# Kernel optimization log

Measured on AMD Instinct MI355X. Metric: run time of the kernel, lower is better.

The kernel has to match this reference:

```python
import jax, jax.numpy as jnp
from jax import lax
import numpy as np

B, N, G, K = 4, 1024, 128, 32
D_MODEL, DEPTH, CLS = 384, 12, 40
D_INNER, D_STATE, D_CONV, DT_RANK = 768, 16, 4, 24
EPS = 1e-5
BN_SCALE = 1.0 / float(np.sqrt(1.0 + EPS))  # eval BN, running_mean=0, running_var=1


def layernorm(x, w, b):
    mu = x.mean(-1, keepdims=True)
    var = ((x - mu) ** 2).mean(-1, keepdims=True)
    return (x - mu) * lax.rsqrt(var + EPS) * w + b


def bn_eval(x, g, b):
    return x * (g * BN_SCALE) + b


def fps(xyz, n):
    Bb, Nn, _ = xyz.shape
    first = jnp.zeros((Bb,), jnp.int32)

    def step(carry, _):
        dmin, last = carry
        p = jnp.take_along_axis(xyz, last[:, None, None], axis=1)  # B,1,3
        dmin = jnp.minimum(dmin, jnp.sum((xyz - p) ** 2, -1))
        nxt = jnp.argmax(dmin, -1).astype(jnp.int32)
        return (dmin, nxt), nxt

    _, rest = lax.scan(step, (jnp.full((Bb, Nn), 1e10, xyz.dtype), first), None, length=n - 1)
    return jnp.concatenate([first[None, :], rest], 0).T  # B,G


def group_points(xyz):
    idx = fps(xyz, G)
    center = jnp.take_along_axis(xyz, idx[:, :, None], axis=1)            # B,G,3
    d2 = jnp.sum((center[:, :, None, :] - xyz[:, None, :, :]) ** 2, -1)   # B,G,N
    _, knn = lax.top_k(-d2, K)                                            # B,G,K
    nb = jax.vmap(lambda p, i: p[i])(xyz, knn)                            # B,G,K,3
    return nb - center[:, :, None, :], center


def encoder(pg, w1, b1, g1, bb1, w2, b2, w3, b3, g2, bb2, w4, b4):
    Bb, Gg, Kk, _ = pg.shape
    f = pg.reshape(Bb * Gg, Kk, 3)
    f = jax.nn.relu(bn_eval(f @ w1.T + b1, g1, bb1))                      # BG,K,128
    f = f @ w2.T + b2                                                     # BG,K,256
    fg = f.max(1, keepdims=True)
    f = jnp.concatenate([jnp.broadcast_to(fg, f.shape), f], -1)           # BG,K,512
    f = jax.nn.relu(bn_eval(f @ w3.T + b3, g2, bb2))
    f = f @ w4.T + b4
    return f.max(1).reshape(Bb, Gg, -1)                                   # B,G,C


def mamba_mixer(x, ipw, cw, cb, xpw, dpw, dpb, A_log, Dp, opw):
    L = x.shape[1]
    xz = x @ ipw.T                                                        # B,L,2*Di
    u, z = jnp.split(xz, 2, -1)
    up = jnp.pad(u, ((0, 0), (D_CONV - 1, 0), (0, 0)))                    # causal depthwise conv
    u = sum(up[:, k:k + L, :] * cw[:, k] for k in range(D_CONV)) + cb
    u = jax.nn.silu(u)
    xdb = u @ xpw.T
    dt, Bm, Cm = jnp.split(xdb, [DT_RANK, DT_RANK + D_STATE], -1)
    dt = jax.nn.softplus(dt @ dpw.T + dpb)                                # B,L,Di
    A = -jnp.exp(A_log)                                                   # Di,Ds

    def step(h, inp):
        dt_t, B_t, C_t, u_t = inp
        h = jnp.exp(dt_t[:, :, None] * A) * h + (dt_t * u_t)[:, :, None] * B_t[:, None, :]
        return h, jnp.einsum('bds,bs->bd', h, C_t)

    h0 = jnp.zeros((x.shape[0], D_INNER, D_STATE), x.dtype)
    _, ys = lax.scan(step, h0, (dt.swapaxes(0, 1), Bm.swapaxes(0, 1), Cm.swapaxes(0, 1), u.swapaxes(0, 1)))
    y = ys.swapaxes(0, 1) + u * Dp
    return (y * jax.nn.silu(z)) @ opw.T


def forward(pts, enc_w1, enc_b1, enc_bn1_g, enc_bn1_b, enc_w2, enc_b2, enc_w3, enc_b3,
            enc_bn2_g, enc_bn2_b, enc_w4, enc_b4, pos_w1, pos_b1, pos_w2, pos_b2,
            ln_w, ln_b, in_proj_w, conv_w, conv_b, x_proj_w, dt_proj_w, dt_proj_b,
            A_log, D_param, out_proj_w, normf_w, normf_b, norm_w, norm_b,
            head_w1, head_b1, head_bn1_g, head_bn1_b, head_w2, head_b2,
            head_bn2_g, head_bn2_b, head_w3, head_b3):
    nb, center = group_points(pts)
    tok = encoder(nb, enc_w1, enc_b1, enc_bn1_g, enc_bn1_b, enc_w2, enc_b2,
                  enc_w3, enc_b3, enc_bn2_g, enc_bn2_b, enc_w4, enc_b4)    # B,G,384
    pos = jax.nn.gelu(center @ pos_w1.T + pos_b1, approximate=False) @ pos_w2.T + pos_b2

    # PointMamba token reordering: sort by center x, y, z and concatenate -> L = 3G
    toks, poss = [], []
    for ax in range(3):
        o = jnp.argsort(center[:, :, ax], axis=-1)[:, :, None]
        toks.append(jnp.take_along_axis(tok, o, axis=1))
        poss.append(jnp.take_along_axis(pos, o, axis=1))
    tok = jnp.concatenate(toks, 1)
    pos = jnp.concatenate(poss, 1)

    h = tok + pos
    res = jnp.zeros_like(h)

    def layer_step(carry, p):
        h, res = carry
        lnw, lnb, ipw, cw, cb, xpw, dpw, dpb, Al, Dp, opw = p
        res = h + res
        x = layernorm(res, lnw, lnb)
        h = mamba_mixer(x, ipw, cw, cb, xpw, dpw, dpb, Al, Dp, opw)
        return (h, res), None

    (h, res), _ = lax.scan(layer_step, (h, res),
                           (ln_w, ln_b, in_proj_w, conv_w, conv_b, x_proj_w,
                            dt_proj_w, dt_proj_b, A_log, D_param, out_proj_w))
    x = layernorm(h + res, normf_w, normf_b)   # MixerModel.norm_f
    x = layernorm(x, norm_w, norm_b)           # PointMamba.norm
    feat = x.mean(1)                           # B,384
    h1 = jax.nn.relu(bn_eval(feat @ head_w1.T + head_b1, head_bn1_g, head_bn1_b))
    h2 = jax.nn.relu(bn_eval(h1 @ head_w2.T + head_b2, head_bn2_g, head_bn2_b))
    return h2 @ head_w3.T + head_b3            # B,CLS


def setup_inputs():
    key = jax.random.key(0)
    ks = iter(jax.random.split(key, 64))

    def rn(shape, s=0.02):
        return jax.random.normal(next(ks), shape, jnp.float32) * s

    inp = dict(
        pts=jax.random.normal(next(ks), (B, N, 3), jnp.float32),
        enc_w1=rn((128, 3), 0.1), enc_b1=jnp.zeros((128,)),
        enc_bn1_g=jnp.ones((128,)), enc_bn1_b=jnp.zeros((128,)),
        enc_w2=rn((256, 128), 0.05), enc_b2=jnp.zeros((256,)),
        enc_w3=rn((512, 512), 0.05), enc_b3=jnp.zeros((512,)),
        enc_bn2_g=jnp.ones((512,)), enc_bn2_b=jnp.zeros((512,)),
        enc_w4=rn((D_MODEL, 512), 0.05), enc_b4=jnp.zeros((D_MODEL,)),
        pos_w1=rn((128, 3), 0.1), pos_b1=jnp.zeros((128,)),
        pos_w2=rn((D_MODEL, 128), 0.05), pos_b2=jnp.zeros((D_MODEL,)),
        ln_w=jnp.ones((DEPTH, D_MODEL)), ln_b=jnp.zeros((DEPTH, D_MODEL)),
        in_proj_w=rn((DEPTH, 2 * D_INNER, D_MODEL)),
        conv_w=rn((DEPTH, D_INNER, D_CONV), 0.2), conv_b=jnp.zeros((DEPTH, D_INNER)),
        x_proj_w=rn((DEPTH, DT_RANK + 2 * D_STATE, D_INNER)),
        dt_proj_w=rn((DEPTH, D_INNER, DT_RANK), 0.1),
        dt_proj_b=jnp.full((DEPTH, D_INNER), -4.6, jnp.float32),
        A_log=jnp.broadcast_to(jnp.log(jnp.arange(1, D_STATE + 1, dtype=jnp.float32)),
                               (DEPTH, D_INNER, D_STATE)).copy(),
        D_param=jnp.ones((DEPTH, D_INNER)),
        out_proj_w=rn((DEPTH, D_MODEL, D_INNER)),
        normf_w=jnp.ones((D_MODEL,)), normf_b=jnp.zeros((D_MODEL,)),
        norm_w=jnp.ones((D_MODEL,)), norm_b=jnp.zeros((D_MODEL,)),
        head_w1=rn((256, D_MODEL), 0.05), head_b1=jnp.zeros((256,)),
        head_bn1_g=jnp.ones((256,)), head_bn1_b=jnp.zeros((256,)),
        head_w2=rn((256, 256), 0.05), head_b2=jnp.zeros((256,)),
        head_bn2_g=jnp.ones((256,)), head_bn2_b=jnp.zeros((256,)),
        head_w3=rn((CLS, 256), 0.05), head_b3=jnp.zeros((CLS,)),
    )
    return inp


def reference(pts, enc_w1, enc_b1, enc_bn1_g, enc_bn1_b, enc_w2, enc_b2, enc_w3, enc_b3,
              enc_bn2_g, enc_bn2_b, enc_w4, enc_b4, pos_w1, pos_b1, pos_w2, pos_b2,
              ln_w, ln_b, in_proj_w, conv_w, conv_b, x_proj_w, dt_proj_w, dt_proj_b,
              A_log, D_param, out_proj_w, normf_w, normf_b, norm_w, norm_b,
              head_w1, head_b1, head_bn1_g, head_bn1_b, head_w2, head_b2,
              head_bn2_g, head_bn2_b, head_w3, head_b3):
    return forward(pts, enc_w1, enc_b1, enc_bn1_g, enc_bn1_b, enc_w2, enc_b2, enc_w3, enc_b3,
                   enc_bn2_g, enc_bn2_b, enc_w4, enc_b4, pos_w1, pos_b1, pos_w2, pos_b2,
                   ln_w, ln_b, in_proj_w, conv_w, conv_b, x_proj_w, dt_proj_w, dt_proj_b,
                   A_log, D_param, out_proj_w, normf_w, normf_b, norm_w, norm_b,
                   head_w1, head_b1, head_bn1_g, head_bn1_b, head_w2, head_b2,
                   head_bn2_g, head_bn2_b, head_w3, head_b3)
```

## Files before the change

### kernel.cpp

```cpp
#include <hip/hip_runtime.h>
#include <hip/hip_bf16.h>

using bf16 = __hip_bfloat16;
using short8  = __attribute__((ext_vector_type(8))) short;
using floatx4 = __attribute__((ext_vector_type(4))) float;
using ull = unsigned long long;

constexpr int Bn = 4, Np = 1024, Gn = 128, Kn = 32;
constexpr int DM = 384, DEPTH = 12, CLSn = 40;
constexpr int DI = 768, DSt = 16, DTR = 24;
constexpr int Ln = 384;
constexpr int NCH = 12, CHS = 32;
constexpr int NLC = 24;
constexpr float EPSf = 1e-5f;
constexpr float BNS = 0.99999500003749968752f;
constexpr float LOG2E = 1.4426950408889634f;

static __device__ __forceinline__ short f2bf(float f){
  bf16 h = __float2bfloat16(f);
  return *reinterpret_cast<short*>(&h);
}
static __device__ __forceinline__ float fsig(float x){ return 1.f/(1.f + __expf(-x)); }
static __device__ __forceinline__ float fsoftplus(float x){
  return fmaxf(x, 0.f) + __logf(1.f + __expf(-fabsf(x)));
}

template<int CTRL>
static __device__ __forceinline__ int dppmov(int x){
  return __builtin_amdgcn_update_dpp(0, x, CTRL, 0xF, 0xF, true);
}
static __device__ __forceinline__ ull redmax64(ull key){
  #define RSTEP(CTRL) { \
    int hi = (int)(unsigned)(key >> 32), lo = (int)(unsigned)key; \
    int h2 = dppmov<CTRL>(hi), l2 = dppmov<CTRL>(lo); \
    ull k2 = ((ull)(unsigned)h2 << 32) | (unsigned)l2; \
    if (k2 > key) key = k2; }
  RSTEP(0x111) RSTEP(0x112) RSTEP(0x114) RSTEP(0x118) RSTEP(0x142) RSTEP(0x143)
  #undef RSTEP
  return key;
}

__global__ __launch_bounds__(64) void fps_kernel(const float* __restrict__ pts,
                                                 float* __restrict__ center){
  int b = blockIdx.x, t = threadIdx.x;
  __shared__ float xs[1024], ys[1024], zs[1024];
  const float* p = pts + (size_t)b * Np * 3;
  float D[16];
  #pragma unroll
  for (int i = 0; i < 16; ++i){
    int n = t + 64*i;
    xs[n] = p[n*3+0]; ys[n] = p[n*3+1]; zs[n] = p[n*3+2];
    D[i] = 1e10f;
  }
  float px = xs[0], py = ys[0], pz = zs[0];
  if (t == 0){
    center[(size_t)(b*Gn)*3+0] = px;
    center[(size_t)(b*Gn)*3+1] = py;
    center[(size_t)(b*Gn)*3+2] = pz;
  }
  for (int it = 1; it < Gn; ++it){
    float v = -1.f; int nbest = t;
    #pragma unroll
    for (int i = 0; i < 16; ++i){
      int n = t + 64*i;
      float dx = __fsub_rn(xs[n], px);
      float dy = __fsub_rn(ys[n], py);
      float dz = __fsub_rn(zs[n], pz);
      float d  = __fadd_rn(__fadd_rn(__fmul_rn(dx,dx), __fmul_rn(dy,dy)), __fmul_rn(dz,dz));
      float dm = fminf(D[i], d); D[i] = dm;
      if (dm > v){ v = dm; nbest = n; }
    }
    ull key = ((ull)__float_as_uint(v) << 32) | (unsigned)(Np-1 - nbest);
    key = redmax64(key);
    int lo63 = __builtin_amdgcn_readlane((int)(unsigned)(key & 0xFFFFFFFFu), 63);
    int wn = Np-1 - lo63;
    wn = min(max(wn, 0), Np-1);
    px = xs[wn]; py = ys[wn]; pz = zs[wn];
    if (t == 0){
      center[(size_t)(b*Gn+it)*3+0] = px;
      center[(size_t)(b*Gn+it)*3+1] = py;
      center[(size_t)(b*Gn+it)*3+2] = pz;
    }
  }
}

__global__ __launch_bounds__(256) void knn_kernel(const float* __restrict__ pts,
                                                  const float* __restrict__ center,
                                                  float* __restrict__ nb){
  int gid = blockIdx.x; int b = gid >> 7;
  __shared__ float d2[1024];
  __shared__ float rv[4]; __shared__ int ri[4];
  int t = threadIdx.x;
  float cx = center[(size_t)gid*3+0], cy = center[(size_t)gid*3+1], cz = center[(size_t)gid*3+2];
  const float* p = pts + (size_t)b * Np * 3;
  for (int n = t; n < Np; n += 256){
    float dx = __fsub_rn(cx, p[n*3+0]);
    float dy = __fsub_rn(cy, p[n*3+1]);
    float dz = __fsub_rn(cz, p[n*3+2]);
    d2[n] = __fadd_rn(__fadd_rn(__fmul_rn(dx,dx), __fmul_rn(dy,dy)), __fmul_rn(dz,dz));
  }
  __syncthreads();
  for (int kk = 0; kk < Kn; ++kk){
    float v = 3e38f; int idx = 0;
    for (int n = t; n < Np; n += 256){
      float d = d2[n];
      if (d < v || (d == v && n < idx)){ v = d; idx = n; }
    }
    ull key = ((ull)(unsigned)(~__float_as_uint(v)) << 32) | (unsigned)(Np-1 - idx);
    key = redmax64(key);
    if ((t & 63) == 63){
      rv[t>>6] = __uint_as_float(~(unsigned)(key >> 32));
      ri[t>>6] = Np-1 - (int)(unsigned)(key & 0xFFFFFFFFu);
    }
    __syncthreads();
    if (t == 0){
      float bv = rv[0]; int bi = ri[0];
      for (int w = 1; w < 4; ++w){
        if (rv[w] < bv || (rv[w] == bv && ri[w] < bi)){ bv = rv[w]; bi = ri[w]; }
      }
      bi = min(max(bi, 0), Np-1);
      nb[((size_t)gid*Kn+kk)*3+0] = __fsub_rn(p[bi*3+0], cx);
      nb[((size_t)gid*Kn+kk)*3+1] = __fsub_rn(p[bi*3+1], cy);
      nb[((size_t)gid*Kn+kk)*3+2] = __fsub_rn(p[bi*3+2], cz);
      d2[bi] = 3e38f;
    }
    __syncthreads();
  }
}

__global__ __launch_bounds__(256) void cvt_bf16(const float* __restrict__ s,
                                                bf16* __restrict__ d, int n){
  int i = (blockIdx.x*256 + threadIdx.x)*4;
  if (i < n){
    float4 v = *(const float4*)(s + i);
    short* o = (short*)d + i;
    o[0] = f2bf(v.x); o[1] = f2bf(v.y); o[2] = f2bf(v.z); o[3] = f2bf(v.w);
  }
}

template<typename AT, typename WT, int ACT, int GATE>
__global__ __launch_bounds__(256) void gemm_mfma(const AT* __restrict__ A, int lda,
                                                 const WT* __restrict__ W,
                                                 const float* __restrict__ bias,
                                                 const float* __restrict__ g,
                                                 const float* __restrict__ bb,
                                                 float* __restrict__ C, int ldc,
                                                 int M, int N, int K){
  __shared__ __align__(16) short As[64*40];
  __shared__ __align__(16) short Ws[64*40];
  int bm = blockIdx.x * 64, bn = blockIdx.y * 64;
  int t = threadIdx.x;
  int row = t >> 2;
  int kseg = (t & 3) * 8;
  int w = t >> 6, lane = t & 63, m16 = lane & 15, q = lane >> 4;
  bool kvec = ((K & 3) == 0) && ((lda & 3) == 0 || sizeof(AT) == 2);
  floatx4 acc[4] = {};
  for (int k0 = 0; k0 < K; k0 += 32){
    if constexpr (GATE){
      const float* Ar = (const float*)A + (size_t)(bm + row)*lda + k0 + kseg;
      float4 y0 = *(const float4*)Ar;
      float4 y1 = *(const float4*)(Ar + 4);
      float4 z0 = *(const float4*)(Ar + 768);
      float4 z1 = *(const float4*)(Ar + 772);
      short* dst = &As[row*40 + kseg];
      dst[0] = f2bf(y0.x * (z0.x * fsig(z0.x)));
      dst[1] = f2bf(y0.y * (z0.y * fsig(z0.y)));
      dst[2] = f2bf(y0.z * (z0.z * fsig(z0.z)));
      dst[3] = f2bf(y0.w * (z0.w * fsig(z0.w)));
      dst[4] = f2bf(y1.x * (z1.x * fsig(z1.x)));
      dst[5] = f2bf(y1.y * (z1.y * fsig(z1.y)));
      dst[6] = f2bf(y1.z * (z1.z * fsig(z1.z)));
      dst[7] = f2bf(y1.w * (z1.w * fsig(z1.w)));
    } else if constexpr (sizeof(AT) == 2){
      *(short8*)&As[row*40 + kseg] =
          *(const short8*)((const short*)A + (size_t)(bm + row)*lda + k0 + kseg);
    } else {
      const float* Ar = (const float*)A + (size_t)(bm + row)*lda;
      short* dst = &As[row*40 + kseg];
      if (kvec && (k0 + kseg + 8 <= K)){
        float4 a0 = *(const float4*)(Ar + k0 + kseg);
        float4 a1 = *(const float4*)(Ar + k0 + kseg + 4);
        dst[0]=f2bf(a0.x); dst[1]=f2bf(a0.y); dst[2]=f2bf(a0.z); dst[3]=f2bf(a0.w);
        dst[4]=f2bf(a1.x); dst[5]=f2bf(a1.y); dst[6]=f2bf(a1.z); dst[7]=f2bf(a1.w);
      } else {
        #pragma unroll
        for (int j = 0; j < 8; ++j){
          int k = k0 + kseg + j;
          dst[j] = (k < K) ? f2bf(Ar[k]) : (short)0;
        }
      }
    }
    if constexpr (sizeof(WT) == 2){
      int n = bn + row;
      short8 v;
      #pragma unroll
      for (int j = 0; j < 8; ++j) v[j] = 0;
      if (n < N) v = *(const short8*)((const short*)W + (size_t)n*K + k0 + kseg);
      *(short8*)&Ws[row*40 + kseg] = v;
    } else {
      int n = bn + row;
      short* dst = &Ws[row*40 + kseg];
      if (n < N && ((K & 3) == 0) && (k0 + kseg + 8 <= K)){
        const float* Wr = (const float*)W + (size_t)n*K + k0 + kseg;
        float4 w0 = *(const float4*)Wr;
        float4 w1 = *(const float4*)(Wr + 4);
        dst[0]=f2bf(w0.x); dst[1]=f2bf(w0.y); dst[2]=f2bf(w0.z); dst[3]=f2bf(w0.w);
        dst[4]=f2bf(w1.x); dst[5]=f2bf(w1.y); dst[6]=f2bf(w1.z); dst[7]=f2bf(w1.w);
      } else {
        #pragma unroll
        for (int j = 0; j < 8; ++j){
          int k = k0 + kseg + j;
          dst[j] = (n < N && k < K) ? f2bf(((const float*)W)[(size_t)n*K + k]) : (short)0;
        }
      }
    }
    __syncthreads();
    short8 af = *(const short8*)&As[(w*16 + m16)*40 + q*8];
    #pragma unroll
    for (int j = 0; j < 4; ++j){
      short8 bfr = *(const short8*)&Ws[(j*16 + m16)*40 + q*8];
      acc[j] = __builtin_amdgcn_mfma_f32_16x16x32_bf16(af, bfr, acc[j], 0, 0, 0);
    }
    __syncthreads();
  }
  #pragma unroll
  for (int j = 0; j < 4; ++j){
    int n = bn + j*16 + m16;
    if (n < N){
      float bv = bias ? bias[n] : 0.f;
      float gv = 0.f, bbv = 0.f;
      if (ACT == 1){ gv = g[n] * BNS; bbv = bb[n]; }
      #pragma unroll
      for (int r = 0; r < 4; ++r){
        int m = bm + w*16 + q*4 + r;
        float v = acc[j][r] + bv;
        if (ACT == 1){ v = v * gv + bbv; v = fmaxf(v, 0.f); }
        C[(size_t)m*ldc + n] = v;
      }
    }
  }
}

__global__ __launch_bounds__(256) void maxk_fg(float* __restrict__ f3in){
  int gg = blockIdx.x; int c = threadIdx.x;
  float m = -3e38f;
  for (int k = 0; k < Kn; ++k) m = fmaxf(m, f3in[((size_t)gg*Kn + k)*512 + 256 + c]);
  for (int k = 0; k < Kn; ++k) f3in[((size_t)gg*Kn + k)*512 + c] = m;
}

__global__ __launch_bounds__(384) void maxk_tok(const float* __restrict__ f4, float* __restrict__ tok){
  int gg = blockIdx.x; int c = threadIdx.x;
  float m = -3e38f;
  for (int k = 0; k < Kn; ++k) m = fmaxf(m, f4[((size_t)gg*Kn + k)*DM + c]);
  tok[(size_t)gg*DM + c] = m;
}

__global__ __launch_bounds__(128) void pos_kernel(const float* __restrict__ center,
                                                  const float* __restrict__ w1, const float* __restrict__ b1,
                                                  const float* __restrict__ w2, const float* __restrict__ b2,
                                                  float* __restrict__ tok){
  int gid = blockIdx.x;
  __shared__ float h1[128]; __shared__ float c3[3];
  int t = threadIdx.x;
  if (t < 3) c3[t] = center[(size_t)gid*3 + t];
  __syncthreads();
  float a = w1[t*3+0]*c3[0] + w1[t*3+1]*c3[1] + w1[t*3+2]*c3[2] + b1[t];
  h1[t] = 0.5f * a * (1.f + erff(a * 0.70710678118654752440f));
  __syncthreads();
  for (int c = t; c < DM; c += 128){
    float s = b2[c];
    for (int j = 0; j < 128; ++j) s += w2[(size_t)c*128 + j] * h1[j];
    tok[(size_t)gid*DM + c] += s;
  }
}

__global__ __launch_bounds__(128) void sort_kernel(const float* __restrict__ center,
                                                   int* __restrict__ order){
  int bax = blockIdx.x; int b = bax / 3, ax = bax % 3;
  __shared__ float key[128];
  int t = threadIdx.x;
  key[t] = center[(size_t)(b*Gn + t)*3 + ax];
  __syncthreads();
  float kt = key[t]; int r = 0;
  for (int j = 0; j < Gn; ++j){
    float kj = key[j];
    r += (kj < kt || (kj == kt && j < t)) ? 1 : 0;
  }
  r = min(max(r, 0), Gn-1);
  order[b*Ln + ax*Gn + r] = t;
}

__global__ __launch_bounds__(256) void build_h(const float* __restrict__ tok,
                        const int* __restrict__ order,
                        float* __restrict__ h, float* __restrict__ res){
  int i = blockIdx.x * blockDim.x + threadIdx.x;
  if (i >= Bn*Ln*DM) return;
  int c = i % DM; int l = (i / DM) % Ln; int b = i / (DM*Ln);
  int src = order[b*Ln + l];
  src = min(max(src, 0), Gn-1);
  h[i] = tok[((size_t)(b*Gn + src))*DM + c];
  res[i] = 0.f;
}

__global__ __launch_bounds__(256) void ln_res_kernel(const float* __restrict__ h,
                                                     float* __restrict__ res,
                                                     bf16* __restrict__ x,
                                                     const float* __restrict__ w,
                                                     const float* __restrict__ bias){
  int wv = threadIdx.x >> 6, ln = threadIdx.x & 63;
  int tokid = blockIdx.x*4 + wv;
  const float* hr = h + (size_t)tokid*DM;
  float* rr = res + (size_t)tokid*DM;
  bf16* xr = x + (size_t)tokid*DM;
  float v[6]; float s = 0.f;
  #pragma unroll
  for (int i = 0; i < 6; ++i){ int c = ln + 64*i; float t = hr[c] + rr[c]; rr[c] = t; v[i] = t; s += t; }
  #pragma unroll
  for (int o = 32; o > 0; o >>= 1) s += __shfl_xor(s, o);
  float mu = s * (1.f/DM);
  float q = 0.f;
  #pragma unroll
  for (int i = 0; i < 6; ++i){ float d = v[i] - mu; q += d*d; }
  #pragma unroll
  for (int o = 32; o > 0; o >>= 1) q += __shfl_xor(q, o);
  float rstd = rsqrtf(q * (1.f/DM) + EPSf);
  #pragma unroll
  for (int i = 0; i < 6; ++i){ int c = ln + 64*i;
    xr[c] = __float2bfloat16((v[i]-mu)*rstd*w[c] + bias[c]); }
}

__global__ __launch_bounds__(256) void conv_fused(const float* __restrict__ xz,
                                                  float* __restrict__ ucv,
                                                  const float* __restrict__ cw,
                                                  const float* __restrict__ cb){
  int blk = blockIdx.x;
  int lc = blk % NLC; int bd = blk / NLC; int dch = bd % 3; int b = bd / 3;
  int t = threadIdx.x; int d = dch*256 + t;
  int l0 = lc*16;
  float w0 = cw[d*4+0], w1 = cw[d*4+1], w2 = cw[d*4+2], w3 = cw[d*4+3];
  float bias = cb[d];
  float u0 = (l0 >= 3) ? xz[((size_t)(b*Ln + l0-3))*1536 + d] : 0.f;
  float u1 = (l0 >= 2) ? xz[((size_t)(b*Ln + l0-2))*1536 + d] : 0.f;
  float u2 = (l0 >= 1) ? xz[((size_t)(b*Ln + l0-1))*1536 + d] : 0.f;
  const float* pin = xz + ((size_t)(b*Ln + l0))*1536 + d;
  float* pout = ucv + ((size_t)(b*Ln + l0))*DI + d;
  float r[16];
  #pragma unroll
  for (int i = 0; i < 16; ++i) r[i] = pin[(size_t)i*1536];
  #pragma unroll
  for (int i = 0; i < 16; ++i){
    float v = u0*w0 + u1*w1 + u2*w2 + r[i]*w3 + bias;
    pout[(size_t)i*DI] = v * fsig(v);
    u0 = u1; u1 = u2; u2 = r[i];
  }
}

__global__ __launch_bounds__(256) void conv_save(const float* __restrict__ xz,
                                                 float* __restrict__ bnd){
  int blk = blockIdx.x;
  int lc = blk % NLC; int bd = blk / NLC; int dch = bd % 3; int b = bd / 3;
  int t = threadIdx.x; int d = dch*256 + t;
  int l0 = lc*16;
  #pragma unroll
  for (int j = 0; j < 3; ++j){
    int l = l0 - 3 + j;
    float v = (l >= 0) ? xz[((size_t)(b*Ln + l))*1536 + d] : 0.f;
    bnd[(((size_t)blk)*3 + j)*256 + t] = v;
  }
}

__global__ __launch_bounds__(256) void conv_apply(float* __restrict__ xz,
                                                  const float* __restrict__ bnd,
                                                  const float* __restrict__ cw,
                                                  const float* __restrict__ cb){
  int blk = blockIdx.x;
  int lc = blk % NLC; int bd = blk / NLC; int dch = bd % 3; int b = bd / 3;
  int t = threadIdx.x; int d = dch*256 + t;
  int l0 = lc*16;
  float w0 = cw[d*4+0], w1 = cw[d*4+1], w2 = cw[d*4+2], w3 = cw[d*4+3];
  float bias = cb[d];
  float u0 = bnd[(((size_t)blk)*3 + 0)*256 + t];
  float u1 = bnd[(((size_t)blk)*3 + 1)*256 + t];
  float u2 = bnd[(((size_t)blk)*3 + 2)*256 + t];
  float* p = xz + ((size_t)(b*Ln + l0))*1536 + d;
  float r[16];
  #pragma unroll
  for (int i = 0; i < 16; ++i) r[i] = p[(size_t)i*1536];
  #pragma unroll
  for (int i = 0; i < 16; ++i){
    float v = u0*w0 + u1*w1 + u2*w2 + r[i]*w3 + bias;
    p[(size_t)i*1536] = v * fsig(v);
    u0 = u1; u1 = u2; u2 = r[i];
  }
}

__global__ __launch_bounds__(256) void scanA_kernel(const float* __restrict__ usrc, int uld,
                                                    const float* __restrict__ xdb,
                                                    const float* __restrict__ dpw,
                                                    const float* __restrict__ dpb,
                                                    const float* __restrict__ A_log,
                                                    float* __restrict__ SB_S,
                                                    float* __restrict__ SB_dt){
  __shared__ float sRow[CHS*56];
  __shared__ float sU[CHS*256];
  int blk = blockIdx.x;
  int c = blk % NCH; int bd = blk / NCH; int dch = bd % 3; int b = bd / 3;
  int t = threadIdx.x; int d = dch*256 + t;
  int l0 = c*CHS;
  for (int i = t; i < CHS*56; i += 256) sRow[i] = xdb[((size_t)(b*Ln + l0))*56 + i];
  const float* up = usrc + ((size_t)(b*Ln + l0))*uld + dch*256;
  #pragma unroll
  for (int i = 0; i < CHS; ++i) sU[i*256 + t] = up[(size_t)i*uld + t];
  float w[DTR];
  const float* wp = dpw + (size_t)d*DTR;
  #pragma unroll
  for (int j = 0; j < DTR; ++j) w[j] = wp[j];
  float a2[DSt], h[DSt];
  const float* ap = A_log + (size_t)d*DSt;
  #pragma unroll
  for (int s = 0; s < DSt; ++s){ a2[s] = -__expf(ap[s]) * LOG2E; h[s] = 0.f; }
  float dbias = dpb[d];
  float sumdt = 0.f;
  __syncthreads();
  for (int i = 0; i < CHS; ++i){
    int ro = i*56;
    float dtr = dbias;
    #pragma unroll
    for (int j = 0; j < DTR; ++j) dtr += w[j] * sRow[ro + j];
    float dtv = fsoftplus(dtr);
    sumdt += dtv;
    float du = dtv * sU[i*256 + t];
    #pragma unroll
    for (int s = 0; s < DSt; ++s)
      h[s] = exp2f(dtv * a2[s]) * h[s] + du * sRow[ro + 24 + s];
  }
  size_t sb = ((size_t)blk*256 + t)*16;
  #pragma unroll
  for (int s = 0; s < DSt; ++s) SB_S[sb + s] = h[s];
  SB_dt[(size_t)blk*256 + t] = sumdt;
}

__global__ __launch_bounds__(256) void scanB_kernel(float* __restrict__ xz,
                                                    const float* __restrict__ usrc, int uld,
                                                    const float* __restrict__ xdb,
                                                    const float* __restrict__ dpw,
                                                    const float* __restrict__ dpb,
                                                    const float* __restrict__ A_log,
                                                    const float* __restrict__ Dp,
                                                    const float* __restrict__ SB_S,
                                                    const float* __restrict__ SB_dt){
  __shared__ float sRow[CHS*56];
  __shared__ float sU[CHS*256];
  int blk = blockIdx.x;
  int c = blk % NCH; int bd = blk / NCH; int dch = bd % 3; int b = bd / 3;
  int t = threadIdx.x; int d = dch*256 + t;
  int l0 = c*CHS;
  for (int i = t; i < CHS*56; i += 256) sRow[i] = xdb[((size_t)(b*Ln + l0))*56 + i];
  const float* up = usrc + ((size_t)(b*Ln + l0))*uld + dch*256;
  #pragma unroll
  for (int i = 0; i < CHS; ++i) sU[i*256 + t] = up[(size_t)i*uld + t];
  float w[DTR];
  const float* wp = dpw + (size_t)d*DTR;
  #pragma unroll
  for (int j = 0; j < DTR; ++j) w[j] = wp[j];
  float a2[DSt], h[DSt];
  const float* ap = A_log + (size_t)d*DSt;
  #pragma unroll
  for (int s = 0; s < DSt; ++s){ a2[s] = -__expf(ap[s]) * LOG2E; h[s] = 0.f; }
  for (int cc = 0; cc < c; ++cc){
    size_t base = (((size_t)bd*NCH + cc)*256 + t)*16;
    float sd = SB_dt[((size_t)bd*NCH + cc)*256 + t];
    #pragma unroll
    for (int s = 0; s < DSt; ++s)
      h[s] = exp2f(sd * a2[s]) * h[s] + SB_S[base + s];
  }
  float dbias = dpb[d];
  float Dd = Dp[d];
  float* ydst = xz + ((size_t)(b*Ln + l0))*1536 + dch*256;
  __syncthreads();
  for (int i = 0; i < CHS; ++i){
    int ro = i*56;
    float dtr = dbias;
    #pragma unroll
    for (int j = 0; j < DTR; ++j) dtr += w[j] * sRow[ro + j];
    float dtv = fsoftplus(dtr);
    float u = sU[i*256 + t];
    float du = dtv * u;
    float yv = 0.f;
    #pragma unroll
    for (int s = 0; s < DSt; ++s){
      h[s] = exp2f(dtv * a2[s]) * h[s] + du * sRow[ro + 24 + s];
      yv += h[s] * sRow[ro + 40 + s];
    }
    ydst[(size_t)i*1536 + t] = yv + u*Dd;
  }
}

__global__ __launch_bounds__(256) void final_ln_kernel(const float* __restrict__ h,
                                                       const float* __restrict__ res,
                                                       const float* w1, const float* b1,
                                                       const float* w2, const float* b2,
                                                       float* __restrict__ x){
  int wv = threadIdx.x >> 6, ln = threadIdx.x & 63;
  int tokid = blockIdx.x*4 + wv;
  const float* hr = h + (size_t)tokid*DM;
  const float* rr = res + (size_t)tokid*DM;
  float* xr = x + (size_t)tokid*DM;
  float v[6]; float s = 0.f;
  #pragma unroll
  for (int i = 0; i < 6; ++i){ int c = ln + 64*i; v[i] = hr[c] + rr[c]; s += v[i]; }
  #pragma unroll
  for (int o = 32; o > 0; o >>= 1) s += __shfl_xor(s, o);
  float mu = s * (1.f/DM); float q = 0.f;
  #pragma unroll
  for (int i = 0; i < 6; ++i){ float dd = v[i]-mu; q += dd*dd; }
  #pragma unroll
  for (int o = 32; o > 0; o >>= 1) q += __shfl_xor(q, o);
  float rstd = rsqrtf(q * (1.f/DM) + EPSf);
  float u[6]; float s2 = 0.f;
  #pragma unroll
  for (int i = 0; i < 6; ++i){ int c = ln + 64*i; u[i] = (v[i]-mu)*rstd*w1[c] + b1[c]; s2 += u[i]; }
  #pragma unroll
  for (int o = 32; o > 0; o >>= 1) s2 += __shfl_xor(s2, o);
  float mu2 = s2 * (1.f/DM); float q2 = 0.f;
  #pragma unroll
  for (int i = 0; i < 6; ++i){ float dd = u[i]-mu2; q2 += dd*dd; }
  #pragma unroll
  for (int o = 32; o > 0; o >>= 1) q2 += __shfl_xor(q2, o);
  float rstd2 = rsqrtf(q2 * (1.f/DM) + EPSf);
  #pragma unroll
  for (int i = 0; i < 6; ++i){ int c = ln + 64*i; xr[c] = (u[i]-mu2)*rstd2*w2[c] + b2[c]; }
}

__global__ __launch_bounds__(384) void head_kernel(const float* __restrict__ x,
    const float* w1, const float* b1, const float* g1, const float* bb1,
    const float* w2, const float* b2, const float* g2, const float* bb2,
    const float* w3, const float* b3, float* __restrict__ out){
  int b = blockIdx.x; int t = threadIdx.x;
  __shared__ float feat[DM]; __shared__ float h1[256]; __shared__ float h2[256];
  float s = 0.f;
  for (int l = 0; l < Ln; ++l) s += x[((size_t)(b*Ln + l))*DM + t];
  feat[t] = s * (1.f/Ln);
  __syncthreads();
  if (t < 256){
    float a = b1[t];
    for (int j = 0; j < DM; ++j) a += w1[(size_t)t*DM + j] * feat[j];
    a = a * (g1[t] * BNS) + bb1[t];
    h1[t] = fmaxf(a, 0.f);
  }
  __syncthreads();
  if (t < 256){
    float a = b2[t];
    for (int j = 0; j < 256; ++j) a += w2[(size_t)t*256 + j] * h1[j];
    a = a * (g2[t] * BNS) + bb2[t];
    h2[t] = fmaxf(a, 0.f);
  }
  __syncthreads();
  if (t < CLSn){
    float a = b3[t];
    for (int j = 0; j < 256; ++j) a += w3[(size_t)t*256 + j] * h2[j];
    out[b*CLSn + t] = a;
  }
}

extern "C" void kernel_launch(void* const* d_in, const int* in_sizes, int n_in,
                              void* d_out, int out_size, void* d_ws, size_t ws_size,
                              hipStream_t stream) {
  if (n_in < 42) return;
  if (out_size < Bn*CLSn) return;
  constexpr size_t WS_FLOATS = 3919936;
  if (ws_size < WS_FLOATS * sizeof(float)) return;
  constexpr size_t MIDF = 5812224;
  constexpr size_t BIGF = 18874368;
  const bool mid = ws_size >= (WS_FLOATS + MIDF) * sizeof(float);
  const bool big = ws_size >= (WS_FLOATS + MIDF + BIGF) * sizeof(float);

  const float* pts       = (const float*)d_in[0];
  const float* enc_w1    = (const float*)d_in[1];  const float* enc_b1    = (const float*)d_in[2];
  const float* enc_bn1_g = (const float*)d_in[3];  const float* enc_bn1_b = (const float*)d_in[4];
  const float* enc_w2    = (const float*)d_in[5];  const float* enc_b2    = (const float*)d_in[6];
  const float* enc_w3    = (const float*)d_in[7];  const float* enc_b3    = (const float*)d_in[8];
  const float* enc_bn2_g = (const float*)d_in[9];  const float* enc_bn2_b = (const float*)d_in[10];
  const float* enc_w4    = (const float*)d_in[11]; const float* enc_b4    = (const float*)d_in[12];
  const float* pos_w1    = (const float*)d_in[13]; const float* pos_b1    = (const float*)d_in[14];
  const float* pos_w2    = (const float*)d_in[15]; const float* pos_b2    = (const float*)d_in[16];
  const float* ln_w      = (const float*)d_in[17]; const float* ln_b      = (const float*)d_in[18];
  const float* in_proj_w = (const float*)d_in[19];
  const float* conv_w    = (const float*)d_in[20]; const float* conv_b    = (const float*)d_in[21];
  const float* x_proj_w  = (const float*)d_in[22];
  const float* dt_proj_w = (const float*)d_in[23]; const float* dt_proj_b = (const float*)d_in[24];
  const float* A_log     = (const float*)d_in[25]; const float* D_param   = (const float*)d_in[26];
  const float* out_proj_w= (const float*)d_in[27];
  const float* normf_w   = (const float*)d_in[28]; const float* normf_b   = (const float*)d_in[29];
  const float* norm_w    = (const float*)d_in[30]; const float* norm_b    = (const float*)d_in[31];
  const float* head_w1   = (const float*)d_in[32]; const float* head_b1   = (const float*)d_in[33];
  const float* head_bn1_g= (const float*)d_in[34]; const float* head_bn1_b= (const float*)d_in[35];
  const float* head_w2   = (const float*)d_in[36]; const float* head_b2   = (const float*)d_in[37];
  const float* head_bn2_g= (const float*)d_in[38]; const float* head_bn2_b= (const float*)d_in[39];
  const float* head_w3   = (const float*)d_in[40]; const float* head_b3   = (const float*)d_in[41];

  float* ws = (float*)d_ws;
  float* hb   = ws;
  float* resb = ws + 589824;
  float* U    = ws + 1179648;
  float* center = U;
  float* nb     = U + 1536;
  float* tok    = U + 50688;
  int*   order  = (int*)(U + 247296);
  float* eb0    = U + 262144;
  float* eb1    = U + 1310720;
  float* xz   = U;
  float* xdb  = U + 2359296;
  bf16*  xb   = (bf16*)(U + 2445312);
  float* SBdt = U + 2445312;
  float* BND  = U + 2482176;
  float* SBS  = hb;
  float* xf   = U;
  float* WB = ws + WS_FLOATS;
  bf16* wb_ip = (bf16*)WB;
  bf16* wb_op = (bf16*)(WB + 3538944);
  bf16* wb_xp = (bf16*)(WB + 5308416);
  bf16* wb_e2 = (bf16*)(WB + 5566464);
  bf16* wb_e3 = (bf16*)(WB + 5582848);
  bf16* wb_e4 = (bf16*)(WB + 5713920);
  float* F3in = WB + MIDF;
  float* F3   = WB + MIDF + 8388608;
  float* F1   = WB + MIDF + 16777216;
  float* F4   = F3in;
  float* ucv  = F3in;

  if (mid){
    cvt_bf16<<<(12*1536*384/4 + 255)/256, 256, 0, stream>>>(in_proj_w, wb_ip, 12*1536*384);
    cvt_bf16<<<(12*384*768/4 + 255)/256, 256, 0, stream>>>(out_proj_w, wb_op, 12*384*768);
    cvt_bf16<<<(12*56*768/4 + 255)/256, 256, 0, stream>>>(x_proj_w, wb_xp, 12*56*768);
    cvt_bf16<<<(256*128/4 + 255)/256, 256, 0, stream>>>(enc_w2, wb_e2, 256*128);
    cvt_bf16<<<(512*512/4 + 255)/256, 256, 0, stream>>>(enc_w3, wb_e3, 512*512);
    cvt_bf16<<<(384*512/4 + 255)/256, 256, 0, stream>>>(enc_w4, wb_e4, 384*512);
  }

  fps_kernel<<<Bn, 64, 0, stream>>>(pts, center);
  knn_kernel<<<Bn*Gn, 256, 0, stream>>>(pts, center, nb);

  if (big){
    gemm_mfma<float,float,1,0><<<dim3(256,2), 256, 0, stream>>>(nb, 3, enc_w1, enc_b1,
        enc_bn1_g, enc_bn1_b, F1, 128, 16384, 128, 3);
    gemm_mfma<float,bf16,0,0><<<dim3(256,4), 256, 0, stream>>>(F1, 128, wb_e2, enc_b2,
        nullptr, nullptr, F3in + 256, 512, 16384, 256, 128);
    maxk_fg<<<512, 256, 0, stream>>>(F3in);
    gemm_mfma<float,bf16,1,0><<<dim3(256,8), 256, 0, stream>>>(F3in, 512, wb_e3, enc_b3,
        enc_bn2_g, enc_bn2_b, F3, 512, 16384, 512, 512);
    gemm_mfma<float,bf16,0,0><<<dim3(256,6), 256, 0, stream>>>(F3, 512, wb_e4, enc_b4,
        nullptr, nullptr, F4, 384, 16384, 384, 512);
    maxk_tok<<<512, 384, 0, stream>>>(F4, tok);
  } else {
    for (int ch = 0; ch < 8; ++ch){
      const float* nb_c = nb + (size_t)ch*2048*3;
      float* tok_c = tok + (size_t)ch*64*DM;
      gemm_mfma<float,float,1,0><<<dim3(32,2), 256, 0, stream>>>(nb_c, 3, enc_w1, enc_b1,
          enc_bn1_g, enc_bn1_b, eb1, 128, 2048, 128, 3);
      if (mid){
        gemm_mfma<float,bf16,0,0><<<dim3(32,4), 256, 0, stream>>>(eb1, 128, wb_e2, enc_b2,
            nullptr, nullptr, eb0 + 256, 512, 2048, 256, 128);
        maxk_fg<<<64, 256, 0, stream>>>(eb0);
        gemm_mfma<float,bf16,1,0><<<dim3(32,8), 256, 0, stream>>>(eb0, 512, wb_e3, enc_b3,
            enc_bn2_g, enc_bn2_b, eb1, 512, 2048, 512, 512);
        gemm_mfma<float,bf16,0,0><<<dim3(32,6), 256, 0, stream>>>(eb1, 512, wb_e4, enc_b4,
            nullptr, nullptr, eb0, 384, 2048, 384, 512);
      } else {
        gemm_mfma<float,float,0,0><<<dim3(32,4), 256, 0, stream>>>(eb1, 128, enc_w2, enc_b2,
            nullptr, nullptr, eb0 + 256, 512, 2048, 256, 128);
        maxk_fg<<<64, 256, 0, stream>>>(eb0);
        gemm_mfma<float,float,1,0><<<dim3(32,8), 256, 0, stream>>>(eb0, 512, enc_w3, enc_b3,
            enc_bn2_g, enc_bn2_b, eb1, 512, 2048, 512, 512);
        gemm_mfma<float,float,0,0><<<dim3(32,6), 256, 0, stream>>>(eb1, 512, enc_w4, enc_b4,
            nullptr, nullptr, eb0, 384, 2048, 384, 512);
      }
      maxk_tok<<<64, 384, 0, stream>>>(eb0, tok_c);
    }
  }

  pos_kernel<<<Bn*Gn, 128, 0, stream>>>(center, pos_w1, pos_b1, pos_w2, pos_b2, tok);
  sort_kernel<<<Bn*3, 128, 0, stream>>>(center, order);
  build_h<<<(Bn*Ln*DM + 255)/256, 256, 0, stream>>>(tok, order, hb, resb);

  for (int l = 0; l < DEPTH; ++l){
    const float* lnw  = ln_w      + (size_t)l*DM;
    const float* lnb  = ln_b      + (size_t)l*DM;
    const float* ipw  = in_proj_w + (size_t)l*1536*DM;
    const float* cw   = conv_w    + (size_t)l*DI*4;
    const float* cb   = conv_b    + (size_t)l*DI;
    const float* xpw  = x_proj_w  + (size_t)l*56*DI;
    const float* dpw  = dt_proj_w + (size_t)l*DI*DTR;
    const float* dpb  = dt_proj_b + (size_t)l*DI;
    const float* Alg  = A_log     + (size_t)l*DI*DSt;
    const float* Dpar = D_param   + (size_t)l*DI;
    const float* opw  = out_proj_w+ (size_t)l*DM*DI;

    ln_res_kernel<<<Bn*Ln/4, 256, 0, stream>>>(hb, resb, xb, lnw, lnb);
    if (mid){
      gemm_mfma<bf16,bf16,0,0><<<dim3(24,24), 256, 0, stream>>>(xb, DM,
          wb_ip + (size_t)l*1536*DM, nullptr, nullptr, nullptr, xz, 1536, Bn*Ln, 1536, DM);
    } else {
      gemm_mfma<bf16,float,0,0><<<dim3(24,24), 256, 0, stream>>>(xb, DM, ipw,
          nullptr, nullptr, nullptr, xz, 1536, Bn*Ln, 1536, DM);
    }
    if (big){
      conv_fused<<<Bn*3*NLC, 256, 0, stream>>>(xz, ucv, cw, cb);
      if (mid)
        gemm_mfma<float,bf16,0,0><<<dim3(24,1), 256, 0, stream>>>(ucv, DI,
            wb_xp + (size_t)l*56*DI, nullptr, nullptr, nullptr, xdb, 56, Bn*Ln, 56, DI);
      else
        gemm_mfma<float,float,0,0><<<dim3(24,1), 256, 0, stream>>>(ucv, DI, xpw,
            nullptr, nullptr, nullptr, xdb, 56, Bn*Ln, 56, DI);
      scanA_kernel<<<Bn*3*NCH, 256, 0, stream>>>(ucv, DI, xdb, dpw, dpb, Alg, SBS, SBdt);
      scanB_kernel<<<Bn*3*NCH, 256, 0, stream>>>(xz, ucv, DI, xdb, dpw, dpb, Alg, Dpar, SBS, SBdt);
    } else {
      conv_save<<<Bn*3*NLC, 256, 0, stream>>>(xz, BND);
      conv_apply<<<Bn*3*NLC, 256, 0, stream>>>(xz, BND, cw, cb);
      if (mid)
        gemm_mfma<float,bf16,0,0><<<dim3(24,1), 256, 0, stream>>>(xz, 1536,
            wb_xp + (size_t)l*56*DI, nullptr, nullptr, nullptr, xdb, 56, Bn*Ln, 56, DI);
      else
        gemm_mfma<float,float,0,0><<<dim3(24,1), 256, 0, stream>>>(xz, 1536, xpw,
            nullptr, nullptr, nullptr, xdb, 56, Bn*Ln, 56, DI);
      scanA_kernel<<<Bn*3*NCH, 256, 0, stream>>>(xz, 1536, xdb, dpw, dpb, Alg, SBS, SBdt);
      scanB_kernel<<<Bn*3*NCH, 256, 0, stream>>>(xz, xz, 1536, xdb, dpw, dpb, Alg, Dpar, SBS, SBdt);
    }
    if (mid){
      gemm_mfma<float,bf16,0,1><<<dim3(24,6), 256, 0, stream>>>(xz, 1536,
          wb_op + (size_t)l*DM*DI, nullptr, nullptr, nullptr, hb, DM, Bn*Ln, DM, DI);
    } else {
      gemm_mfma<float,float,0,1><<<dim3(24,6), 256, 0, stream>>>(xz, 1536, opw,
          nullptr, nullptr, nullptr, hb, DM, Bn*Ln, DM, DI);
    }
  }

  final_ln_kernel<<<Bn*Ln/4, 256, 0, stream>>>(hb, resb, normf_w, normf_b, norm_w, norm_b, xf);
  head_kernel<<<Bn, 384, 0, stream>>>(xf, head_w1, head_b1, head_bn1_g, head_bn1_b,
                                      head_w2, head_b2, head_bn2_g, head_bn2_b,
                                      head_w3, head_b3, (float*)d_out);
}
```

Baseline: 1.786 ms.

## Add 128x128 MFMA GEMM tile, keep FPS points in registers, parameterize scan output

```diff
diff --git a/kernel.cpp b/kernel.cpp
--- a/kernel.cpp
+++ b/kernel.cpp
@@ -45,13 +45,16 @@
   int b = blockIdx.x, t = threadIdx.x;
   __shared__ float xs[1024], ys[1024], zs[1024];
   const float* p = pts + (size_t)b * Np * 3;
-  float D[16];
+  float X[16], Y[16], Z[16], D[16];
   #pragma unroll
   for (int i = 0; i < 16; ++i){
     int n = t + 64*i;
-    xs[n] = p[n*3+0]; ys[n] = p[n*3+1]; zs[n] = p[n*3+2];
+    float a = p[n*3+0], c = p[n*3+1], e = p[n*3+2];
+    X[i] = a; Y[i] = c; Z[i] = e;
+    xs[n] = a; ys[n] = c; zs[n] = e;
     D[i] = 1e10f;
   }
+  __syncthreads();
   float px = xs[0], py = ys[0], pz = zs[0];
   if (t == 0){
     center[(size_t)(b*Gn)*3+0] = px;
@@ -62,13 +65,12 @@
     float v = -1.f; int nbest = t;
     #pragma unroll
     for (int i = 0; i < 16; ++i){
-      int n = t + 64*i;
-      float dx = __fsub_rn(xs[n], px);
-      float dy = __fsub_rn(ys[n], py);
-      float dz = __fsub_rn(zs[n], pz);
+      float dx = __fsub_rn(X[i], px);
+      float dy = __fsub_rn(Y[i], py);
+      float dz = __fsub_rn(Z[i], pz);
       float d  = __fadd_rn(__fadd_rn(__fmul_rn(dx,dx), __fmul_rn(dy,dy)), __fmul_rn(dz,dz));
       float dm = fminf(D[i], d); D[i] = dm;
-      if (dm > v){ v = dm; nbest = n; }
+      if (dm > v){ v = dm; nbest = t + 64*i; }
     }
     ull key = ((ull)__float_as_uint(v) << 32) | (unsigned)(Np-1 - nbest);
     key = redmax64(key);
@@ -138,12 +140,12 @@
   }
 }
 
-template<typename AT, typename WT, int ACT, int GATE>
+template<typename AT, typename WT, int ACT, int MODE>
 __global__ __launch_bounds__(256) void gemm_mfma(const AT* __restrict__ A, int lda,
                                                  const WT* __restrict__ W,
                                                  const float* __restrict__ bias,
-                                                 const float* __restrict__ g,
-                                                 const float* __restrict__ bb,
+                                                 const float* __restrict__ gz,
+                                                 const float* __restrict__ bbp,
                                                  float* __restrict__ C, int ldc,
                                                  int M, int N, int K){
   __shared__ __align__(16) short As[64*40];
@@ -156,21 +158,15 @@
   bool kvec = ((K & 3) == 0) && ((lda & 3) == 0 || sizeof(AT) == 2);
   floatx4 acc[4] = {};
   for (int k0 = 0; k0 < K; k0 += 32){
-    if constexpr (GATE){
-      const float* Ar = (const float*)A + (size_t)(bm + row)*lda + k0 + kseg;
-      float4 y0 = *(const float4*)Ar;
-      float4 y1 = *(const float4*)(Ar + 4);
-      float4 z0 = *(const float4*)(Ar + 768);
-      float4 z1 = *(const float4*)(Ar + 772);
+    if constexpr (MODE == 1){
+      const float* Yr = (const float*)A + (size_t)(bm + row)*lda + k0 + kseg;
+      const float* Zr = gz + (size_t)(bm + row)*1536 + 768 + k0 + kseg;
+      float y[8], z[8];
+      *(float4*)&y[0] = *(const float4*)Yr;  *(float4*)&y[4] = *(const float4*)(Yr + 4);
+      *(float4*)&z[0] = *(const float4*)Zr;  *(float4*)&z[4] = *(const float4*)(Zr + 4);
       short* dst = &As[row*40 + kseg];
-      dst[0] = f2bf(y0.x * (z0.x * fsig(z0.x)));
-      dst[1] = f2bf(y0.y * (z0.y * fsig(z0.y)));
-      dst[2] = f2bf(y0.z * (z0.z * fsig(z0.z)));
-      dst[3] = f2bf(y0.w * (z0.w * fsig(z0.w)));
-      dst[4] = f2bf(y1.x * (z1.x * fsig(z1.x)));
-      dst[5] = f2bf(y1.y * (z1.y * fsig(z1.y)));
-      dst[6] = f2bf(y1.z * (z1.z * fsig(z1.z)));
-      dst[7] = f2bf(y1.w * (z1.w * fsig(z1.w)));
+      #pragma unroll
+      for (int jj = 0; jj < 8; ++jj) dst[jj] = f2bf(y[jj] * (z[jj] * fsig(z[jj])));
     } else if constexpr (sizeof(AT) == 2){
       *(short8*)&As[row*40 + kseg] =
           *(const short8*)((const short*)A + (size_t)(bm + row)*lda + k0 + kseg);
@@ -229,11 +225,94 @@
     if (n < N){
       float bv = bias ? bias[n] : 0.f;
       float gv = 0.f, bbv = 0.f;
-      if (ACT == 1){ gv = g[n] * BNS; bbv = bb[n]; }
+      if (ACT == 1){ gv = gz[n] * BNS; bbv = bbp[n]; }
       #pragma unroll
       for (int r = 0; r < 4; ++r){
         int m = bm + w*16 + q*4 + r;
         float v = acc[j][r] + bv;
+        if (ACT == 1){ v = v * gv + bbv; v = fmaxf(v, 0.f); }
+        C[(size_t)m*ldc + n] = v;
+      }
+    }
+  }
+}
+
+template<typename AT, typename WT, int ACT>
+__global__ __launch_bounds__(256) void gemm_mfma_128(const AT* __restrict__ A, int lda,
+                                                     const WT* __restrict__ W,
+                                                     const float* __restrict__ bias,
+                                                     const float* __restrict__ g,
+                                                     const float* __restrict__ bb,
+                                                     float* __restrict__ C, int ldc,
+                                                     int M, int N, int K){
+  __shared__ __align__(16) short As[128*40];
+  __shared__ __align__(16) short Ws[128*40];
+  int bm = blockIdx.x * 128, bn = blockIdx.y * 128;
+  int t = threadIdx.x;
+  int row = t >> 1;
+  int kseg = (t & 1) * 16;
+  int w = t >> 6, lane = t & 63, m16 = lane & 15, q = lane >> 4;
+  int wr = (w >> 1)*64, wc = (w & 1)*64;
+  floatx4 acc[4][4] = {};
+  for (int k0 = 0; k0 < K; k0 += 32){
+    if constexpr (sizeof(AT) == 2){
+      const short* Ar = (const short*)A + (size_t)(bm + row)*lda + k0 + kseg;
+      *(short8*)&As[row*40 + kseg]     = *(const short8*)Ar;
+      *(short8*)&As[row*40 + kseg + 8] = *(const short8*)(Ar + 8);
+    } else {
+      const float* Ar = (const float*)A + (size_t)(bm + row)*lda + k0 + kseg;
+      float4 a0 = *(const float4*)Ar;
+      float4 a1 = *(const float4*)(Ar + 4);
+      float4 a2 = *(const float4*)(Ar + 8);
+      float4 a3 = *(const float4*)(Ar + 12);
+      short* dst = &As[row*40 + kseg];
+      dst[0]=f2bf(a0.x); dst[1]=f2bf(a0.y); dst[2]=f2bf(a0.z); dst[3]=f2bf(a0.w);
+      dst[4]=f2bf(a1.x); dst[5]=f2bf(a1.y); dst[6]=f2bf(a1.z); dst[7]=f2bf(a1.w);
+      dst[8]=f2bf(a2.x); dst[9]=f2bf(a2.y); dst[10]=f2bf(a2.z); dst[11]=f2bf(a2.w);
+      dst[12]=f2bf(a3.x); dst[13]=f2bf(a3.y); dst[14]=f2bf(a3.z); dst[15]=f2bf(a3.w);
+    }
+    if constexpr (sizeof(WT) == 2){
+      const short* Wr = (const short*)W + (size_t)(bn + row)*K + k0 + kseg;
+      *(short8*)&Ws[row*40 + kseg]     = *(const short8*)Wr;
+      *(short8*)&Ws[row*40 + kseg + 8] = *(const short8*)(Wr + 8);
+    } else {
+      const float* Wr = (const float*)W + (size_t)(bn + row)*K + k0 + kseg;
+      float4 w0 = *(const float4*)Wr;
+      float4 w1 = *(const float4*)(Wr + 4);
+      float4 w2 = *(const float4*)(Wr + 8);
+      float4 w3 = *(const float4*)(Wr + 12);
+      short* dst = &Ws[row*40 + kseg];
+      dst[0]=f2bf(w0.x); dst[1]=f2bf(w0.y); dst[2]=f2bf(w0.z); dst[3]=f2bf(w0.w);
+      dst[4]=f2bf(w1.x); dst[5]=f2bf(w1.y); dst[6]=f2bf(w1.z); dst[7]=f2bf(w1.w);
+      dst[8]=f2bf(w2.x); dst[9]=f2bf(w2.y); dst[10]=f2bf(w2.z); dst[11]=f2bf(w2.w);
+      dst[12]=f2bf(w3.x); dst[13]=f2bf(w3.y); dst[14]=f2bf(w3.z); dst[15]=f2bf(w3.w);
+    }
+    __syncthreads();
+    short8 af[4];
+    #pragma unroll
+    for (int i = 0; i < 4; ++i)
+      af[i] = *(const short8*)&As[(wr + i*16 + m16)*40 + q*8];
+    #pragma unroll
+    for (int j = 0; j < 4; ++j){
+      short8 bw = *(const short8*)&Ws[(wc + j*16 + m16)*40 + q*8];
+      #pragma unroll
+      for (int i = 0; i < 4; ++i)
+        acc[i][j] = __builtin_amdgcn_mfma_f32_16x16x32_bf16(af[i], bw, acc[i][j], 0, 0, 0);
+    }
+    __syncthreads();
+  }
+  #pragma unroll
+  for (int j = 0; j < 4; ++j){
+    int n = bn + wc + j*16 + m16;
+    float bv = bias ? bias[n] : 0.f;
+    float gv = 0.f, bbv = 0.f;
+    if (ACT == 1){ gv = g[n] * BNS; bbv = bb[n]; }
+    #pragma unroll
+    for (int i = 0; i < 4; ++i){
+      #pragma unroll
+      for (int r = 0; r < 4; ++r){
+        int m = bm + wr + i*16 + q*4 + r;
+        float v = acc[i][j][r] + bv;
         if (ACT == 1){ v = v * gv + bbv; v = fmaxf(v, 0.f); }
         C[(size_t)m*ldc + n] = v;
       }
@@ -440,7 +519,7 @@
   SB_dt[(size_t)blk*256 + t] = sumdt;
 }
 
-__global__ __launch_bounds__(256) void scanB_kernel(float* __restrict__ xz,
+__global__ __launch_bounds__(256) void scanB_kernel(float* __restrict__ ydst_base, int ys,
                                                     const float* __restrict__ usrc, int uld,
                                                     const float* __restrict__ xdb,
                                                     const float* __restrict__ dpw,
@@ -476,7 +555,7 @@
   }
   float dbias = dpb[d];
   float Dd = Dp[d];
-  float* ydst = xz + ((size_t)(b*Ln + l0))*1536 + dch*256;
+  float* ydst = ydst_base + ((size_t)(b*Ln + l0))*ys + dch*256;
   __syncthreads();
   for (int i = 0; i < CHS; ++i){
     int ro = i*56;
@@ -492,7 +571,7 @@
       h[s] = exp2f(dtv * a2[s]) * h[s] + du * sRow[ro + 24 + s];
       yv += h[s] * sRow[ro + 40 + s];
     }
-    ydst[(size_t)i*1536 + t] = yv + u*Dd;
+    ydst[(size_t)i*ys + t] = yv + u*Dd;
   }
 }
 
@@ -612,9 +691,9 @@
   float* xz   = U;
   float* xdb  = U + 2359296;
   bf16*  xb   = (bf16*)(U + 2445312);
-  float* SBdt = U + 2445312;
+  float* SBdt_s = U + 2445312;
   float* BND  = U + 2482176;
-  float* SBS  = hb;
+  float* SBS_s  = hb;
   float* xf   = U;
   float* WB = ws + WS_FLOATS;
   bf16* wb_ip = (bf16*)WB;
@@ -628,6 +707,8 @@
   float* F1   = WB + MIDF + 16777216;
   float* F4   = F3in;
   float* ucv  = F3in;
+  float* SBS_b  = F3;
+  float* SBdt_b = F1;
 
   if (mid){
     cvt_bf16<<<(12*1536*384/4 + 255)/256, 256, 0, stream>>>(in_proj_w, wb_ip, 12*1536*384);
@@ -644,12 +725,12 @@
   if (big){
     gemm_mfma<float,float,1,0><<<dim3(256,2), 256, 0, stream>>>(nb, 3, enc_w1, enc_b1,
         enc_bn1_g, enc_bn1_b, F1, 128, 16384, 128, 3);
-    gemm_mfma<float,bf16,0,0><<<dim3(256,4), 256, 0, stream>>>(F1, 128, wb_e2, enc_b2,
+    gemm_mfma_128<float,bf16,0><<<dim3(128,2), 256, 0, stream>>>(F1, 128, wb_e2, enc_b2,
         nullptr, nullptr, F3in + 256, 512, 16384, 256, 128);
     maxk_fg<<<512, 256, 0, stream>>>(F3in);
-    gemm_mfma<float,bf16,1,0><<<dim3(256,8), 256, 0, stream>>>(F3in, 512, wb_e3, enc_b3,
+    gemm_mfma_128<float,bf16,1><<<dim3(128,4), 256, 0, stream>>>(F3in, 512, wb_e3, enc_b3,
         enc_bn2_g, enc_bn2_b, F3, 512, 16384, 512, 512);
-    gemm_mfma<float,bf16,0,0><<<dim3(256,6), 256, 0, stream>>>(F3, 512, wb_e4, enc_b4,
+    gemm_mfma_128<float,bf16,0><<<dim3(128,3), 256, 0, stream>>>(F3, 512, wb_e4, enc_b4,
         nullptr, nullptr, F4, 384, 16384, 384, 512);
     maxk_tok<<<512, 384, 0, stream>>>(F4, tok);
   } else {
@@ -659,20 +740,20 @@
       gemm_mfma<float,float,1,0><<<dim3(32,2), 256, 0, stream>>>(nb_c, 3, enc_w1, enc_b1,
           enc_bn1_g, enc_bn1_b, eb1, 128, 2048, 128, 3);
       if (mid){
-        gemm_mfma<float,bf16,0,0><<<dim3(32,4), 256, 0, stream>>>(eb1, 128, wb_e2, enc_b2,
+        gemm_mfma_128<float,bf16,0><<<dim3(16,2), 256, 0, stream>>>(eb1, 128, wb_e2, enc_b2,
             nullptr, nullptr, eb0 + 256, 512, 2048, 256, 128);
         maxk_fg<<<64, 256, 0, stream>>>(eb0);
-        gemm_mfma<float,bf16,1,0><<<dim3(32,8), 256, 0, stream>>>(eb0, 512, wb_e3, enc_b3,
+        gemm_mfma_128<float,bf16,1><<<dim3(16,4), 256, 0, stream>>>(eb0, 512, wb_e3, enc_b3,
             enc_bn2_g, enc_bn2_b, eb1, 512, 2048, 512, 512);
-        gemm_mfma<float,bf16,0,0><<<dim3(32,6), 256, 0, stream>>>(eb1, 512, wb_e4, enc_b4,
+        gemm_mfma_128<float,bf16,0><<<dim3(16,3), 256, 0, stream>>>(eb1, 512, wb_e4, enc_b4,
             nullptr, nullptr, eb0, 384, 2048, 384, 512);
       } else {
-        gemm_mfma<float,float,0,0><<<dim3(32,4), 256, 0, stream>>>(eb1, 128, enc_w2, enc_b2,
+        gemm_mfma_128<float,float,0><<<dim3(16,2), 256, 0, stream>>>(eb1, 128, enc_w2, enc_b2,
             nullptr, nullptr, eb0 + 256, 512, 2048, 256, 128);
         maxk_fg<<<64, 256, 0, stream>>>(eb0);
-        gemm_mfma<float,float,1,0><<<dim3(32,8), 256, 0, stream>>>(eb0, 512, enc_w3, enc_b3,
+        gemm_mfma_128<float,float,1><<<dim3(16,4), 256, 0, stream>>>(eb0, 512, enc_w3, enc_b3,
             enc_bn2_g, enc_bn2_b, eb1, 512, 2048, 512, 512);
-        gemm_mfma<float,float,0,0><<<dim3(32,6), 256, 0, stream>>>(eb1, 512, enc_w4, enc_b4,
+        gemm_mfma_128<float,float,0><<<dim3(16,3), 256, 0, stream>>>(eb1, 512, enc_w4, enc_b4,
             nullptr, nullptr, eb0, 384, 2048, 384, 512);
       }
       maxk_tok<<<64, 384, 0, stream>>>(eb0, tok_c);
@@ -698,10 +779,10 @@
 
     ln_res_kernel<<<Bn*Ln/4, 256, 0, stream>>>(hb, resb, xb, lnw, lnb);
     if (mid){
-      gemm_mfma<bf16,bf16,0,0><<<dim3(24,24), 256, 0, stream>>>(xb, DM,
+      gemm_mfma_128<bf16,bf16,0><<<dim3(12,12), 256, 0, stream>>>(xb, DM,
           wb_ip + (size_t)l*1536*DM, nullptr, nullptr, nullptr, xz, 1536, Bn*Ln, 1536, DM);
     } else {
-      gemm_mfma<bf16,float,0,0><<<dim3(24,24), 256, 0, stream>>>(xb, DM, ipw,
+      gemm_mfma_128<bf16,float,0><<<dim3(12,12), 256, 0, stream>>>(xb, DM, ipw,
           nullptr, nullptr, nullptr, xz, 1536, Bn*Ln, 1536, DM);
     }
     if (big){
@@ -712,8 +793,9 @@
       else
         gemm_mfma<float,float,0,0><<<dim3(24,1), 256, 0, stream>>>(ucv, DI, xpw,
             nullptr, nullptr, nullptr, xdb, 56, Bn*Ln, 56, DI);
-      scanA_kernel<<<Bn*3*NCH, 256, 0, stream>>>(ucv, DI, xdb, dpw, dpb, Alg, SBS, SBdt);
-      scanB_kernel<<<Bn*3*NCH, 256, 0, stream>>>(xz, ucv, DI, xdb, dpw, dpb, Alg, Dpar, SBS, SBdt);
+      scanA_kernel<<<Bn*3*NCH, 256, 0, stream>>>(ucv, DI, xdb, dpw, dpb, Alg, SBS_b, SBdt_b);
+      scanB_kernel<<<Bn*3*NCH, 256, 0, stream>>>(xz, 1536, ucv, DI,
+          xdb, dpw, dpb, Alg, Dpar, SBS_b, SBdt_b);
     } else {
       conv_save<<<Bn*3*NLC, 256, 0, stream>>>(xz, BND);
       conv_apply<<<Bn*3*NLC, 256, 0, stream>>>(xz, BND, cw, cb);
@@ -723,15 +805,16 @@
       else
         gemm_mfma<float,float,0,0><<<dim3(24,1), 256, 0, stream>>>(xz, 1536, xpw,
             nullptr, nullptr, nullptr, xdb, 56, Bn*Ln, 56, DI);
-      scanA_kernel<<<Bn*3*NCH, 256, 0, stream>>>(xz, 1536, xdb, dpw, dpb, Alg, SBS, SBdt);
-      scanB_kernel<<<Bn*3*NCH, 256, 0, stream>>>(xz, xz, 1536, xdb, dpw, dpb, Alg, Dpar, SBS, SBdt);
+      scanA_kernel<<<Bn*3*NCH, 256, 0, stream>>>(xz, 1536, xdb, dpw, dpb, Alg, SBS_s, SBdt_s);
+      scanB_kernel<<<Bn*3*NCH, 256, 0, stream>>>(xz, 1536, xz, 1536,
+          xdb, dpw, dpb, Alg, Dpar, SBS_s, SBdt_s);
     }
     if (mid){
       gemm_mfma<float,bf16,0,1><<<dim3(24,6), 256, 0, stream>>>(xz, 1536,
-          wb_op + (size_t)l*DM*DI, nullptr, nullptr, nullptr, hb, DM, Bn*Ln, DM, DI);
+          wb_op + (size_t)l*DM*DI, nullptr, xz, nullptr, hb, DM, Bn*Ln, DM, DI);
     } else {
       gemm_mfma<float,float,0,1><<<dim3(24,6), 256, 0, stream>>>(xz, 1536, opw,
-          nullptr, nullptr, nullptr, hb, DM, Bn*Ln, DM, DI);
+          nullptr, xz, nullptr, hb, DM, Bn*Ln, DM, DI);
     }
   }
 
```

New measurement: 1.809 ms. About the same (+1.3%).
